# Kernel tuning notes

Measured on AMD Instinct MI355X. Metric: run time of the kernel, lower is better.

## Reference

```python
import jax, jax.numpy as jnp
import numpy as np

EMBED_DIM = 512
NUM_HEADS = 8
TGT_LEN = 1024
BSZ = 16


def setup_inputs() -> dict:
    key = jax.random.key(0)
    ks = jax.random.split(key, 6)
    E = EMBED_DIM
    query = jax.random.normal(ks[0], (TGT_LEN, BSZ, E), jnp.float32)
    i_proj = jax.random.normal(ks[1], (3 * E,), jnp.float32)
    # xavier_uniform-ish scale for (3E, E)
    lim = (6.0 / (3 * E + E)) ** 0.5
    in_proj_weight = jax.random.uniform(ks[2], (3 * E, E), jnp.float32, -lim, lim)
    in_proj_bias = jnp.zeros((3 * E,), jnp.float32)
    lim2 = (6.0 / (2 * E)) ** 0.5
    out_w = jax.random.uniform(ks[3], (E, E), jnp.float32, -lim2, lim2)
    out_b = jnp.zeros((E,), jnp.float32)
    bias_k = jax.random.normal(ks[4], (1, 1, E), jnp.float32)
    bias_v = jax.random.normal(ks[5], (1, 1, E), jnp.float32)
    return dict(query=query, i_proj=i_proj, in_proj_weight=in_proj_weight,
                in_proj_bias=in_proj_bias, out_w=out_w, out_b=out_b,
                bias_k=bias_k, bias_v=bias_v)


def reference(query, i_proj, in_proj_weight, in_proj_bias, out_w, out_b, bias_k, bias_v):
    # qkv_same path: key = value = query (self-attention)
    T, B, E = query.shape
    H = NUM_HEADS
    hd = E // H
    scaling = hd ** -0.5
    # per-call weight mutation: every 3rd column replaced by i_proj
    w = in_proj_weight.at[:, ::3].set(i_proj[:, None])
    qkv = jnp.einsum('tbe,fe->tbf', query, w) + in_proj_bias  # (T, B, 3E)
    q, k, v = jnp.split(qkv, 3, axis=-1)
    q = q * scaling
    k = jnp.concatenate([k, jnp.broadcast_to(bias_k, (1, B, E))], axis=0)  # (T+1, B, E)
    v = jnp.concatenate([v, jnp.broadcast_to(bias_v, (1, B, E))], axis=0)
    S = k.shape[0]
    q = q.reshape(T, B * H, hd).transpose(1, 0, 2)  # (B*H, T, hd)
    k = k.reshape(S, B * H, hd).transpose(1, 0, 2)  # (B*H, S, hd)
    v = v.reshape(S, B * H, hd).transpose(1, 0, 2)
    aw = jnp.einsum('nth,nsh->nts', q, k)  # (B*H, T, S)
    # global min-max normalization over the entire score tensor (not softmax)
    mn = jnp.min(aw)
    mx = jnp.max(aw)
    aw = (aw - mn) / (mx - mn)
    attn = jnp.einsum('nts,nsh->nth', aw, v)  # (B*H, T, hd)
    attn = attn.transpose(1, 0, 2).reshape(T, B, E)
    attn = attn @ out_w.T + out_b  # out_proj
    aw_avg = aw.reshape(B, H, T, S).sum(axis=1) / H  # (B, T, S)
    wq, wk, wv = jnp.split(w, 3, axis=0)
    w_ret = jnp.stack([wq.T, wk.T, wv.T], axis=0)  # (3, E, E)
    return attn, aw_avg, w_ret
```

## Files before the change

### kernel.cpp

```cpp
#include <hip/hip_runtime.h>
#include <hip/hip_bf16.h>
#include <stdint.h>

typedef __bf16 bf16;
typedef __bf16 bf16x8 __attribute__((ext_vector_type(8)));
typedef __bf16 bf16x4 __attribute__((ext_vector_type(4)));
typedef float  f32x4  __attribute__((ext_vector_type(4)));

#define MFMA_BF16(a,b,c) __builtin_amdgcn_mfma_f32_16x16x32_bf16((a),(b),(c),0,0,0)

#define WS_QBF_IN  0L
#define WS_WBF     16777216L
#define WS_OUTWBF  18350080L
#define WS_Q       18874368L
#define WS_K       35651584L
#define WS_V       52428800L
#define WS_VT      69206016L
#define WS_AWLAST  85983232L
#define WS_VCS     86507520L
#define WS_MM      86540288L
#define WS_KT      86540544L
#define WS_KTV     103317760L

__device__ __forceinline__ void gload16(const void* g, void* l) {
  __builtin_amdgcn_global_load_lds((const __attribute__((address_space(1))) uint32_t*)g,
                                   (__attribute__((address_space(3))) uint32_t*)l, 16, 0, 0);
}
__device__ __forceinline__ unsigned ordf(float x) {
  unsigned b = __float_as_uint(x);
  return (b & 0x80000000u) ? ~b : (b | 0x80000000u);
}
__device__ __forceinline__ float deordf(unsigned u) {
  unsigned b = (u & 0x80000000u) ? (u ^ 0x80000000u) : ~u;
  return __uint_as_float(b);
}

__global__ __launch_bounds__(256) void cvt_query_kernel(const float* __restrict__ in,
                                                        bf16* __restrict__ out) {
  long i = (long)blockIdx.x * 256 + threadIdx.x;
  for (; i < 2097152L; i += (long)gridDim.x * 256) {
    float4 v = ((const float4*)in)[i];
    bf16x4 o; o[0] = (bf16)v.x; o[1] = (bf16)v.y; o[2] = (bf16)v.z; o[3] = (bf16)v.w;
    ((bf16x4*)out)[i] = o;
  }
}

__global__ __launch_bounds__(256) void prep_weights_kernel(
    const float* __restrict__ in_w, const float* __restrict__ i_proj,
    const float* __restrict__ out_w, bf16* __restrict__ w_bf,
    bf16* __restrict__ outw_bf, float* __restrict__ w_ret,
    unsigned* __restrict__ mm) {
  long idx = (long)blockIdx.x * 256 + threadIdx.x;
  if (idx == 0) { mm[0] = 0xFFFFFFFFu; mm[1] = 0u; }
  if (idx < 786432L) {
    int f = (int)(idx >> 9), e = (int)(idx & 511);
    float val = (e % 3 == 0) ? i_proj[f] : in_w[idx];
    w_bf[idx] = (bf16)val;
    w_ret[(long)(f >> 9) * 262144 + (long)e * 512 + (f & 511)] = val;
  } else if (idx < 1048576L) {
    long j = idx - 786432L;
    outw_bf[j] = (bf16)out_w[j];
  }
}

#define PIPE_STAGE(Abase_, Bbase_, kk_, buf_)                                      \
  do {                                                                             \
    _Pragma("unroll")                                                              \
    for (int i_ = 0; i_ < 4; ++i_) {                                               \
      int c_ = tid + i_ * 256;                                                     \
      int row_ = c_ >> 3;                                                          \
      int cc_ = (c_ & 7) ^ (row_ & 7);                                             \
      gload16((Abase_) + (long)row_ * 512 + (kk_) + cc_ * 8,                       \
              (char*)aT[buf_] + (i_ * 256 + w * 64) * 16);                         \
      gload16((Bbase_) + (long)row_ * 512 + (kk_) + cc_ * 8,                       \
              (char*)bT[buf_] + (i_ * 256 + w * 64) * 16);                         \
    }                                                                              \
  } while (0)

#define PIPE_COMPUTE(buf_)                                                         \
  do {                                                                             \
    _Pragma("unroll")                                                              \
    for (int ks_ = 0; ks_ < 2; ++ks_) {                                            \
      bf16x8 af[4], bfr[4];                                                        \
      _Pragma("unroll")                                                            \
      for (int mi_ = 0; mi_ < 4; ++mi_) {                                          \
        int r_ = rm + mi_ * 16 + l15;                                              \
        int p_ = (ks_ * 4 + l4) ^ (r_ & 7);                                        \
        af[mi_] = *(const bf16x8*)((const char*)aT[buf_] + r_ * 128 + p_ * 16);    \
      }                                                                            \
      _Pragma("unroll")                                                            \
      for (int ni_ = 0; ni_ < 4; ++ni_) {                                          \
        int r_ = cn + ni_ * 16 + l15;                                              \
        int p_ = (ks_ * 4 + l4) ^ (r_ & 7);                                        \
        bfr[ni_] = *(const bf16x8*)((const char*)bT[buf_] + r_ * 128 + p_ * 16);   \
      }                                                                            \
      _Pragma("unroll")                                                            \
      for (int mi_ = 0; mi_ < 4; ++mi_)                                            \
        _Pragma("unroll")                                                          \
        for (int ni_ = 0; ni_ < 4; ++ni_)                                          \
          acc[mi_][ni_] = MFMA_BF16(af[mi_], bfr[ni_], acc[mi_][ni_]);             \
    }                                                                              \
  } while (0)

template <int MODE>
__global__ __launch_bounds__(256, 2) void gemm_kernel(
    const bf16* __restrict__ A, const bf16* __restrict__ B,
    const float* __restrict__ bias,
    bf16* __restrict__ q_out, bf16* __restrict__ k_out, bf16* __restrict__ v_out,
    float* __restrict__ outC) {
  __shared__ __align__(16) bf16 aT[2][128 * 64];
  __shared__ __align__(16) bf16 bT[2][128 * 64];
  const int tid = threadIdx.x;
  const int lane = tid & 63, w = tid >> 6;
  const int l15 = lane & 15, l4 = lane >> 4;
  const long r0 = (long)blockIdx.y * 128;
  const long f0 = (long)blockIdx.x * 128;
  const int rm = (w >> 1) * 64, cn = (w & 1) * 64;
  const bf16* Ab = A + r0 * 512;
  const bf16* Bb = B + f0 * 512;
  f32x4 acc[4][4] = {};

  PIPE_STAGE(Ab, Bb, 0, 0);
  PIPE_STAGE(Ab, Bb, 64, 1);
  asm volatile("s_waitcnt vmcnt(8)" ::: "memory");
  __builtin_amdgcn_s_barrier();
  __builtin_amdgcn_sched_barrier(0);
#pragma unroll
  for (int k = 0; k < 8; ++k) {
    PIPE_COMPUTE(k & 1);
    __builtin_amdgcn_s_barrier();
    __builtin_amdgcn_sched_barrier(0);
    if (k + 2 < 8) PIPE_STAGE(Ab, Bb, (k + 2) * 64, k & 1);
    if (k + 1 < 8) {
      if (k + 2 < 8) asm volatile("s_waitcnt vmcnt(8)" ::: "memory");
      else           asm volatile("s_waitcnt vmcnt(0)" ::: "memory");
      __builtin_amdgcn_s_barrier();
      __builtin_amdgcn_sched_barrier(0);
    }
  }
#pragma unroll
  for (int mi = 0; mi < 4; ++mi)
#pragma unroll
    for (int ni = 0; ni < 4; ++ni)
#pragma unroll
      for (int r = 0; r < 4; ++r) {
        long row = r0 + rm + mi * 16 + l4 * 4 + r;
        int f = (int)f0 + cn + ni * 16 + l15;
        float val = acc[mi][ni][r] + bias[f];
        if (MODE == 0) {
          int t = (int)(row >> 4), b = (int)(row & 15);
          int which = f >> 9, hh = (f >> 6) & 7, d = f & 63;
          long off = ((long)(b * 8 + hh) * 1024 + t) * 64 + d;
          if (which == 0)      q_out[off] = (bf16)(val * 0.125f);
          else if (which == 1) k_out[off] = (bf16)val;
          else                 v_out[off] = (bf16)val;
        } else {
          outC[row * 512 + f] = val;
        }
      }
}

__global__ __launch_bounds__(256, 2) void awsum_gemm_kernel(
    const bf16* __restrict__ q_bf, const bf16* __restrict__ k_bf,
    bf16* __restrict__ aw_raw, unsigned* __restrict__ mm) {
  __shared__ __align__(16) bf16 aT[2][128 * 64];
  __shared__ __align__(16) bf16 bT[2][128 * 64];
  const int tid = threadIdx.x;
  const int lane = tid & 63, w = tid >> 6;
  const int l15 = lane & 15, l4 = lane >> 4;
  const int bid = blockIdx.x;
  const int xcd = bid & 7, slot = bid >> 3;
  const int b = xcd * 2 + (slot >> 6);
  const int rest = slot & 63;
  const int t0 = (rest >> 3) * 128;
  const int s0 = (rest & 7) * 128;
  const int rm = (w >> 1) * 64, cn = (w & 1) * 64;
  const bf16* qb = q_bf + (long)b * 8 * 65536 + (long)t0 * 64;
  const bf16* kb = k_bf + (long)b * 8 * 65536 + (long)s0 * 64;

  f32x4 acc[4][4] = {};
  f32x4 snap[4][4] = {};
  float vmin = 1e30f, vmax = -1e30f;

#define AWS_STAGE13(h_, buf_)                                                      \
  do {                                                                             \
    _Pragma("unroll")                                                              \
    for (int i_ = 0; i_ < 4; ++i_) {                                               \
      int c_ = tid + i_ * 256;                                                     \
      int row_ = c_ >> 3;                                                          \
      int cc_ = (c_ & 7) ^ (row_ & 7);                                             \
      gload16(qb + (long)(h_) * 65536 + (long)row_ * 64 + cc_ * 8,                 \
              (char*)aT[buf_] + (i_ * 256 + w * 64) * 16);                         \
      gload16(kb + (long)(h_) * 65536 + (long)row_ * 64 + cc_ * 8,                 \
              (char*)bT[buf_] + (i_ * 256 + w * 64) * 16);                         \
    }                                                                              \
  } while (0)

  AWS_STAGE13(0, 0);
  AWS_STAGE13(1, 1);
  asm volatile("s_waitcnt vmcnt(8)" ::: "memory");
  __builtin_amdgcn_s_barrier();
  __builtin_amdgcn_sched_barrier(0);
#pragma unroll
  for (int h = 0; h < 8; ++h) {
    PIPE_COMPUTE(h & 1);
#pragma unroll
    for (int mi = 0; mi < 4; ++mi)
#pragma unroll
      for (int ni = 0; ni < 4; ++ni) {
        f32x4 d = acc[mi][ni] - snap[mi][ni];
#pragma unroll
        for (int r = 0; r < 4; ++r) {
          vmin = fminf(vmin, d[r]);
          vmax = fmaxf(vmax, d[r]);
        }
        snap[mi][ni] = acc[mi][ni];
      }
    __builtin_amdgcn_s_barrier();
    __builtin_amdgcn_sched_barrier(0);
    if (h + 2 < 8) AWS_STAGE13(h + 2, h & 1);
    if (h + 1 < 8) {
      if (h + 2 < 8) asm volatile("s_waitcnt vmcnt(8)" ::: "memory");
      else           asm volatile("s_waitcnt vmcnt(0)" ::: "memory");
      __builtin_amdgcn_s_barrier();
      __builtin_amdgcn_sched_barrier(0);
    }
  }
#pragma unroll
  for (int mi = 0; mi < 4; ++mi)
#pragma unroll
    for (int ni = 0; ni < 4; ++ni)
#pragma unroll
      for (int r = 0; r < 4; ++r) {
        int t = t0 + rm + mi * 16 + l4 * 4 + r;
        int s = s0 + cn + ni * 16 + l15;
        aw_raw[((long)b * 1024 + t) * 1024 + s] = (bf16)acc[mi][ni][r];
      }
#pragma unroll
  for (int off = 32; off; off >>= 1) {
    vmin = fminf(vmin, __shfl_xor(vmin, off));
    vmax = fmaxf(vmax, __shfl_xor(vmax, off));
  }
  if (lane == 0) { atomicMin(&mm[0], ordf(vmin)); atomicMax(&mm[1], ordf(vmax)); }
}

__global__ __launch_bounds__(256) void transpose_kv_kernel(
    const bf16* __restrict__ k_bf, const bf16* __restrict__ v_bf,
    bf16* __restrict__ kT, bf16* __restrict__ vT) {
  const bf16* src = blockIdx.z ? v_bf : k_bf;
  bf16* dst = blockIdx.z ? vT : kT;
  const int n = blockIdx.y;
  const long s0 = (long)blockIdx.x * 64;
  __shared__ __align__(16) bf16 tile[64][72];
  const int tid = threadIdx.x;
  const int row = tid >> 3, cc = tid & 7;
#pragma unroll
  for (int it = 0; it < 2; ++it) {
    int r = row + it * 32;
    bf16x8 vv = *(const bf16x8*)(src + ((long)n * 1024 + s0 + r) * 64 + cc * 8);
    *(bf16x8*)&tile[r][cc * 8] = vv;
  }
  __syncthreads();
#pragma unroll
  for (int it = 0; it < 2; ++it) {
    int d = row + it * 32;
    bf16x8 ov;
#pragma unroll
    for (int j = 0; j < 8; ++j) ov[j] = tile[cc * 8 + j][d];
    *(bf16x8*)(dst + ((long)n * 64 + d) * 1024 + s0 + cc * 8) = ov;
  }
}

__global__ __launch_bounds__(256) void vcolsum_kernel(const bf16* __restrict__ vT,
                                                      const float* __restrict__ bias_v,
                                                      float* __restrict__ vcs) {
  const int n = blockIdx.x, h = n & 7;
  const int d = threadIdx.x >> 2, q = threadIdx.x & 3;
  float acc = 0.f;
  const bf16* row = vT + (long)n * 65536 + (long)d * 1024 + q * 256;
#pragma unroll 4
  for (int j = 0; j < 32; ++j) {
    bf16x8 v = *(const bf16x8*)(row + j * 8);
#pragma unroll
    for (int e = 0; e < 8; ++e) acc += (float)v[e];
  }
  __shared__ float red[256];
  red[threadIdx.x] = acc;
  __syncthreads();
  if (q == 0)
    vcs[n * 64 + d] = red[d * 4] + red[d * 4 + 1] + red[d * 4 + 2] + red[d * 4 + 3] +
                      bias_v[h * 64 + d];
}

__global__ __launch_bounds__(256) void ktv_kernel(const bf16* __restrict__ kT,
                                                  const bf16* __restrict__ vT,
                                                  bf16* __restrict__ ktvT) {
  const int n = blockIdx.x;
  const int tid = threadIdx.x;
  const int lane = tid & 63, w = tid >> 6;
  const int l15 = lane & 15, l4 = lane >> 4;
  const int wr = w >> 1, wc = w & 1;
  f32x4 acc[2][2] = {};
  const bf16* kbase = kT + (long)n * 65536;
  const bf16* vbase = vT + (long)n * 65536;
  for (int s0 = 0; s0 < 1024; s0 += 32) {
    bf16x8 af[2], bfr[2];
#pragma unroll
    for (int mi = 0; mi < 2; ++mi)
      af[mi] = *(const bf16x8*)(kbase + (long)(wr * 32 + mi * 16 + l15) * 1024 + s0 + l4 * 8);
#pragma unroll
    for (int ni = 0; ni < 2; ++ni)
      bfr[ni] = *(const bf16x8*)(vbase + (long)(wc * 32 + ni * 16 + l15) * 1024 + s0 + l4 * 8);
#pragma unroll
    for (int mi = 0; mi < 2; ++mi)
#pragma unroll
      for (int ni = 0; ni < 2; ++ni)
        acc[mi][ni] = MFMA_BF16(af[mi], bfr[ni], acc[mi][ni]);
  }
#pragma unroll
  for (int mi = 0; mi < 2; ++mi)
#pragma unroll
    for (int ni = 0; ni < 2; ++ni)
#pragma unroll
      for (int r = 0; r < 4; ++r) {
        int d = wr * 32 + mi * 16 + l4 * 4 + r;
        int dp = wc * 32 + ni * 16 + l15;
        ktvT[(long)n * 4096 + dp * 64 + d] = (bf16)acc[mi][ni][r];
      }
}

__global__ __launch_bounds__(256) void qattn_kernel(
    const bf16* __restrict__ q_bf, const bf16* __restrict__ ktvT,
    const float* __restrict__ aw_last, const float* __restrict__ vcs,
    const float* __restrict__ bias_v, const unsigned* __restrict__ mm,
    bf16* __restrict__ A2) {
  const int tid = threadIdx.x;
  const int lane = tid & 63, w = tid >> 6;
  const int l15 = lane & 15, l4 = lane >> 4;
  const int t0 = blockIdx.x * 64;
  const int h = blockIdx.y * 4 + w;
  const int b = blockIdx.z;
  const long n = (long)b * 8 + h;
  f32x4 acc[4][4] = {};
  const bf16* qbase = q_bf + (n * 1024 + t0) * 64;
  const bf16* kbase = ktvT + (long)n * 4096;
#pragma unroll
  for (int kk = 0; kk < 64; kk += 32) {
    bf16x8 af[4], bfr[4];
#pragma unroll
    for (int mi = 0; mi < 4; ++mi)
      af[mi] = *(const bf16x8*)(qbase + (mi * 16 + l15) * 64 + kk + l4 * 8);
#pragma unroll
    for (int ni = 0; ni < 4; ++ni)
      bfr[ni] = *(const bf16x8*)(kbase + (ni * 16 + l15) * 64 + kk + l4 * 8);
#pragma unroll
    for (int mi = 0; mi < 4; ++mi)
#pragma unroll
      for (int ni = 0; ni < 4; ++ni)
        acc[mi][ni] = MFMA_BF16(af[mi], bfr[ni], acc[mi][ni]);
  }
  float mn = deordf(mm[0]), mx = deordf(mm[1]);
  float a = 1.f / (mx - mn), c = -mn * a;
#pragma unroll
  for (int mi = 0; mi < 4; ++mi)
#pragma unroll
    for (int r = 0; r < 4; ++r) {
      int t = t0 + mi * 16 + l4 * 4 + r;
      float alast = a * aw_last[n * 1024 + t];
#pragma unroll
      for (int ni = 0; ni < 4; ++ni) {
        int dp = ni * 16 + l15;
        float val = a * acc[mi][ni][r] + alast * bias_v[h * 64 + dp] + c * vcs[n * 64 + dp];
        A2[((long)t * 16 + b) * 512 + h * 64 + dp] = (bf16)val;
      }
    }
}

__global__ __launch_bounds__(256) void bias_col_kernel(const bf16* __restrict__ q_bf,
                                                       const float* __restrict__ bias_k,
                                                       float* __restrict__ aw_last,
                                                       unsigned* __restrict__ mm) {
  const int n = blockIdx.y, h = n & 7;
  const int t = blockIdx.x * 256 + threadIdx.x;
  float acc = 0.f;
  const bf16* qrow = q_bf + ((long)n * 1024 + t) * 64;
#pragma unroll
  for (int j = 0; j < 8; ++j) {
    bf16x8 qv = *(const bf16x8*)(qrow + j * 8);
#pragma unroll
    for (int e = 0; e < 8; ++e) acc += (float)qv[e] * bias_k[h * 64 + j * 8 + e];
  }
  aw_last[(long)n * 1024 + t] = acc;
  float vmin = acc, vmax = acc;
#pragma unroll
  for (int off = 32; off; off >>= 1) {
    vmin = fminf(vmin, __shfl_xor(vmin, off));
    vmax = fmaxf(vmax, __shfl_xor(vmax, off));
  }
  if ((threadIdx.x & 63) == 0) { atomicMin(&mm[0], ordf(vmin)); atomicMax(&mm[1], ordf(vmax)); }
}

__global__ __launch_bounds__(256) void rescale_kernel(const bf16* __restrict__ aw_raw,
                                                      float* __restrict__ aw_out,
                                                      const float* __restrict__ aw_last,
                                                      const unsigned* __restrict__ mm) {
  long idx = (long)blockIdx.x * 256 + threadIdx.x;
  float mn = deordf(mm[0]), mx = deordf(mm[1]);
  float a = 1.f / (mx - mn), c = -mn * a;
  int s = (int)(idx % 1025);
  long bt = idx / 1025;
  float v;
  if (s < 1024) {
    v = (float)aw_raw[bt * 1024 + s];
  } else {
    int b = (int)(bt >> 10), t = (int)(bt & 1023);
    v = 0.f;
#pragma unroll
    for (int h = 0; h < 8; ++h) v += aw_last[(long)(b * 8 + h) * 1024 + t];
  }
  aw_out[idx] = fmaf(a, v * 0.125f, c);
}

extern "C" void kernel_launch(void* const* d_in, const int* in_sizes, int n_in,
                              void* d_out, int out_size, void* d_ws, size_t ws_size,
                              hipStream_t stream) {
  const float* query  = (const float*)d_in[0];
  const float* i_proj = (const float*)d_in[1];
  const float* in_w   = (const float*)d_in[2];
  const float* in_b   = (const float*)d_in[3];
  const float* out_w  = (const float*)d_in[4];
  const float* out_b  = (const float*)d_in[5];
  const float* bias_k = (const float*)d_in[6];
  const float* bias_v = (const float*)d_in[7];
  float* out = (float*)d_out;

  char* ws = (char*)d_ws;
  bf16* qbf_in = (bf16*)(ws + WS_QBF_IN);
  bf16* w_bf   = (bf16*)(ws + WS_WBF);
  bf16* outwbf = (bf16*)(ws + WS_OUTWBF);
  bf16* q_bf   = (bf16*)(ws + WS_Q);
  bf16* k_bf   = (bf16*)(ws + WS_K);
  bf16* v_bf   = (bf16*)(ws + WS_V);
  bf16* vT     = (bf16*)(ws + WS_VT);
  bf16* kT     = (bf16*)(ws + WS_KT);
  bf16* ktvT   = (bf16*)(ws + WS_KTV);
  bf16* aw_raw = (bf16*)(ws + WS_V);
  float* aw_last = (float*)(ws + WS_AWLAST);
  float* vcs     = (float*)(ws + WS_VCS);
  unsigned* mm   = (unsigned*)(ws + WS_MM);
  bf16* A2 = qbf_in;

  float* out_attn  = out;
  float* out_awavg = out + 8388608L;
  float* out_wret  = out + 25182208L;

  cvt_query_kernel<<<2048, 256, 0, stream>>>(query, qbf_in);
  prep_weights_kernel<<<4096, 256, 0, stream>>>(in_w, i_proj, out_w, w_bf, outwbf, out_wret, mm);
  gemm_kernel<0><<<dim3(12, 128), 256, 0, stream>>>(qbf_in, w_bf, in_b, q_bf, k_bf, v_bf, nullptr);
  transpose_kv_kernel<<<dim3(16, 128, 2), 256, 0, stream>>>(k_bf, v_bf, kT, vT);
  vcolsum_kernel<<<128, 256, 0, stream>>>(vT, bias_v, vcs);
  bias_col_kernel<<<dim3(4, 128), 256, 0, stream>>>(q_bf, bias_k, aw_last, mm);
  ktv_kernel<<<128, 256, 0, stream>>>(kT, vT, ktvT);
  awsum_gemm_kernel<<<1024, 256, 0, stream>>>(q_bf, k_bf, aw_raw, mm);
  rescale_kernel<<<65600, 256, 0, stream>>>(aw_raw, out_awavg, aw_last, mm);
  qattn_kernel<<<dim3(16, 2, 16), 256, 0, stream>>>(q_bf, ktvT, aw_last, vcs, bias_v, mm, A2);
  gemm_kernel<1><<<dim3(4, 128), 256, 0, stream>>>(A2, outwbf, out_b, nullptr, nullptr, nullptr, out_attn);
}
```

Baseline: 306.7 us.

## Give each wave private LDS buffers to drop block barriers in awsum GEMM

Restructures the per-head QK^T score GEMM so each wave stages its own 64x64 Q and K tiles into a private LDS region. The pipeline splits each head's K dimension into two 32-wide stages, and synchronization uses only per-wave waitcnt instead of block-wide s_barrier. The block tile changes from 128x128 shared by four waves to 64x256, with each wave owning a 64-column strip. Q tiles are now loaded redundantly by all four waves. That trades more global/L2 traffic and a smaller per-stage K slice for removing cross-wave barrier stalls.

```diff
diff --git a/kernel.cpp b/kernel.cpp
--- a/kernel.cpp
+++ b/kernel.cpp
@@ -163,8 +163,7 @@
 __global__ __launch_bounds__(256, 2) void awsum_gemm_kernel(
     const bf16* __restrict__ q_bf, const bf16* __restrict__ k_bf,
     bf16* __restrict__ aw_raw, unsigned* __restrict__ mm) {
-  __shared__ __align__(16) bf16 aT[2][128 * 64];
-  __shared__ __align__(16) bf16 bT[2][128 * 64];
+  __shared__ __align__(16) char wlds[4][16384];
   const int tid = threadIdx.x;
   const int lane = tid & 63, w = tid >> 6;
   const int l15 = lane & 15, l4 = lane >> 4;
@@ -172,58 +171,78 @@
   const int xcd = bid & 7, slot = bid >> 3;
   const int b = xcd * 2 + (slot >> 6);
   const int rest = slot & 63;
-  const int t0 = (rest >> 3) * 128;
-  const int s0 = (rest & 7) * 128;
-  const int rm = (w >> 1) * 64, cn = (w & 1) * 64;
-  const bf16* qb = q_bf + (long)b * 8 * 65536 + (long)t0 * 64;
-  const bf16* kb = k_bf + (long)b * 8 * 65536 + (long)s0 * 64;
+  const int t0 = (rest >> 2) * 64;
+  const int s0w = (rest & 3) * 256 + w * 64;
+  char* lA = wlds[w];
+  char* lB = wlds[w] + 8192;
 
   f32x4 acc[4][4] = {};
   f32x4 snap[4][4] = {};
   float vmin = 1e30f, vmax = -1e30f;
 
-#define AWS_STAGE13(h_, buf_)                                                      \
-  do {                                                                             \
-    _Pragma("unroll")                                                              \
-    for (int i_ = 0; i_ < 4; ++i_) {                                               \
-      int c_ = tid + i_ * 256;                                                     \
-      int row_ = c_ >> 3;                                                          \
-      int cc_ = (c_ & 7) ^ (row_ & 7);                                             \
-      gload16(qb + (long)(h_) * 65536 + (long)row_ * 64 + cc_ * 8,                 \
-              (char*)aT[buf_] + (i_ * 256 + w * 64) * 16);                         \
-      gload16(kb + (long)(h_) * 65536 + (long)row_ * 64 + cc_ * 8,                 \
-              (char*)bT[buf_] + (i_ * 256 + w * 64) * 16);                         \
-    }                                                                              \
+#define WAVE_STAGE(k_, buf_)                                                          \
+  do {                                                                                \
+    const int hh_ = (k_) >> 1, kh_ = ((k_) & 1) * 32;                                 \
+    const bf16* qb_ = q_bf + ((long)(b * 8 + hh_) * 1024 + t0) * 64 + kh_;            \
+    const bf16* kb_ = k_bf + ((long)(b * 8 + hh_) * 1024 + s0w) * 64 + kh_;           \
+    _Pragma("unroll")                                                                 \
+    for (int i_ = 0; i_ < 4; ++i_) {                                                  \
+      int ci_ = lane + i_ * 64;                                                       \
+      int row_ = ci_ >> 2, cc_ = ci_ & 3;                                             \
+      int cc2_ = cc_ ^ ((row_ >> 1) & 3);                                             \
+      gload16(qb_ + (long)row_ * 64 + cc2_ * 8, lA + (buf_) * 4096 + i_ * 1024);      \
+      gload16(kb_ + (long)row_ * 64 + cc2_ * 8, lB + (buf_) * 4096 + i_ * 1024);      \
+    }                                                                                 \
   } while (0)
 
-  AWS_STAGE13(0, 0);
-  AWS_STAGE13(1, 1);
-  asm volatile("s_waitcnt vmcnt(8)" ::: "memory");
-  __builtin_amdgcn_s_barrier();
-  __builtin_amdgcn_sched_barrier(0);
-#pragma unroll
-  for (int h = 0; h < 8; ++h) {
-    PIPE_COMPUTE(h & 1);
-#pragma unroll
-    for (int mi = 0; mi < 4; ++mi)
-#pragma unroll
-      for (int ni = 0; ni < 4; ++ni) {
-        f32x4 d = acc[mi][ni] - snap[mi][ni];
-#pragma unroll
-        for (int r = 0; r < 4; ++r) {
-          vmin = fminf(vmin, d[r]);
-          vmax = fmaxf(vmax, d[r]);
+#define WAVE_COMPUTE(buf_)                                                            \
+  do {                                                                                \
+    bf16x8 af[4], bfr[4];                                                             \
+    _Pragma("unroll")                                                                 \
+    for (int mi_ = 0; mi_ < 4; ++mi_) {                                               \
+      int r_ = mi_ * 16 + l15;                                                        \
+      int p_ = l4 ^ ((r_ >> 1) & 3);                                                  \
+      af[mi_] = *(const bf16x8*)(lA + (buf_) * 4096 + r_ * 64 + p_ * 16);             \
+    }                                                                                 \
+    _Pragma("unroll")                                                                 \
+    for (int ni_ = 0; ni_ < 4; ++ni_) {                                               \
+      int r_ = ni_ * 16 + l15;                                                        \
+      int p_ = l4 ^ ((r_ >> 1) & 3);                                                  \
+      bfr[ni_] = *(const bf16x8*)(lB + (buf_) * 4096 + r_ * 64 + p_ * 16);            \
+    }                                                                                 \
+    _Pragma("unroll")                                                                 \
+    for (int mi_ = 0; mi_ < 4; ++mi_)                                                 \
+      _Pragma("unroll")                                                               \
+      for (int ni_ = 0; ni_ < 4; ++ni_)                                               \
+        acc[mi_][ni_] = MFMA_BF16(af[mi_], bfr[ni_], acc[mi_][ni_]);                  \
+  } while (0)
+
+  WAVE_STAGE(0, 0);
+  WAVE_STAGE(1, 1);
+#pragma unroll
+  for (int k = 0; k < 16; ++k) {
+    if (k < 15) asm volatile("s_waitcnt vmcnt(8)" ::: "memory");
+    else        asm volatile("s_waitcnt vmcnt(0)" ::: "memory");
+    __builtin_amdgcn_sched_barrier(0);
+    WAVE_COMPUTE(k & 1);
+    if (k & 1) {
+#pragma unroll
+      for (int mi = 0; mi < 4; ++mi)
+#pragma unroll
+        for (int ni = 0; ni < 4; ++ni) {
+          f32x4 d = acc[mi][ni] - snap[mi][ni];
+#pragma unroll
+          for (int r = 0; r < 4; ++r) {
+            vmin = fminf(vmin, d[r]);
+            vmax = fmaxf(vmax, d[r]);
+          }
+          snap[mi][ni] = acc[mi][ni];
         }
-        snap[mi][ni] = acc[mi][ni];
-      }
-    __builtin_amdgcn_s_barrier();
-    __builtin_amdgcn_sched_barrier(0);
-    if (h + 2 < 8) AWS_STAGE13(h + 2, h & 1);
-    if (h + 1 < 8) {
-      if (h + 2 < 8) asm volatile("s_waitcnt vmcnt(8)" ::: "memory");
-      else           asm volatile("s_waitcnt vmcnt(0)" ::: "memory");
-      __builtin_amdgcn_s_barrier();
+    }
+    if (k + 2 < 16) {
+      asm volatile("s_waitcnt lgkmcnt(0)" ::: "memory");
       __builtin_amdgcn_sched_barrier(0);
+      WAVE_STAGE(k + 2, k & 1);
     }
   }
 #pragma unroll
@@ -232,8 +251,8 @@
     for (int ni = 0; ni < 4; ++ni)
 #pragma unroll
       for (int r = 0; r < 4; ++r) {
-        int t = t0 + rm + mi * 16 + l4 * 4 + r;
-        int s = s0 + cn + ni * 16 + l15;
+        int t = t0 + mi * 16 + l4 * 4 + r;
+        int s = s0w + ni * 16 + l15;
         aw_raw[((long)b * 1024 + t) * 1024 + s] = (bf16)acc[mi][ni][r];
       }
 #pragma unroll
@@ -242,6 +261,8 @@
     vmax = fmaxf(vmax, __shfl_xor(vmax, off));
   }
   if (lane == 0) { atomicMin(&mm[0], ordf(vmin)); atomicMax(&mm[1], ordf(vmax)); }
+#undef WAVE_STAGE
+#undef WAVE_COMPUTE
 }
 
 __global__ __launch_bounds__(256) void transpose_kv_kernel(
```

Result: no change. 309.4 us (+0.9%).
